# Kernel tuning notes

Measured on AMD Instinct MI355X. Metric: run time of the kernel, lower is better.

The kernel has to match this reference:

```python
import jax, jax.numpy as jnp
import numpy as np

IN_CH = 128
HID = 64
EPS = 1e-5
N_NODES = 20000
E_UND = 80000


def _build_line_graph(edge_index, num_nodes):
    # dedupe to unique undirected edges (src<dst); line-graph nodes = these edges
    src = np.asarray(edge_index[0]); dst = np.asarray(edge_index[1])
    m = src < dst
    u, v = src[m], dst[m]
    key = u.astype(np.int64) * num_nodes + v.astype(np.int64)
    _, first = np.unique(key, return_index=True)
    u, v = u[first], v[first]
    E = u.shape[0]
    # incidence lists grouped by node; all ordered pairs of co-incident edges
    nodes = np.concatenate([u, v])
    eids = np.concatenate([np.arange(E), np.arange(E)])
    order = np.argsort(nodes, kind="stable")
    nodes_s, eids_s = nodes[order], eids[order]
    counts = np.bincount(nodes_s, minlength=num_nodes)
    offsets = np.concatenate([np.zeros(1, np.int64), np.cumsum(counts)])
    grp_start = offsets[nodes_s]
    reps = counts[nodes_s]
    total = int(reps.sum())
    starts = np.cumsum(reps) - reps
    idx = np.arange(total) - np.repeat(starts, reps) + np.repeat(grp_start, reps)
    row = np.repeat(eids_s, reps); col = eids_s[idx]
    keep = row != col
    return np.stack([u, v]), np.stack([row[keep], col[keep]])


def _gcn_conv(x, src, dst, W, b):
    # PyG GCNConv: add self loops, symmetric D^-1/2 (A+I) D^-1/2 normalization
    N = x.shape[0]
    sl = jnp.arange(N)
    s = jnp.concatenate([src, sl]); d = jnp.concatenate([dst, sl])
    deg = jax.ops.segment_sum(jnp.ones(s.shape[0], x.dtype), d, num_segments=N)
    dinv = jax.lax.rsqrt(jnp.maximum(deg, 1.0))
    h = x @ W
    msg = h[s] * (dinv[s] * dinv[d])[:, None]
    return jax.ops.segment_sum(msg, d, num_segments=N) + b


def _edge_scores(line_x, lsrc, ldst, W1, b1, gamma1, beta1, W2, b2):
    h = _gcn_conv(line_x, lsrc, ldst, W1, b1)
    mu = h.mean(0); var = h.var(0)  # BatchNorm1d, training-mode batch stats
    h = jax.nn.relu(gamma1 * (h - mu) * jax.lax.rsqrt(var + EPS) + beta1)
    return jax.nn.sigmoid(_gcn_conv(h, lsrc, ldst, W2, b2))[:, 0]


def _cluster(clean, topk_idx, num_nodes):
    ti = np.asarray(topk_idx)
    sel_src = np.asarray(clean[0])[ti]; sel_dst = np.asarray(clean[1])[ti]
    n2c = np.arange(num_nodes)
    rev = sel_dst[::-1]
    _, fi = np.unique(rev, return_index=True)
    last = sel_dst.shape[0] - 1 - fi
    n2c[sel_dst[last]] = sel_src[last]
    uniq = np.unique(n2c)
    M = int(uniq.shape[0])
    old_to_new = np.full(num_nodes, -1, np.int64)
    old_to_new[uniq] = np.arange(M)
    return old_to_new[n2c], uniq, M


def _make_graph():
    rng = np.random.default_rng(0)
    a = rng.integers(0, N_NODES, E_UND)
    off = rng.integers(1, N_NODES, E_UND)
    b = (a + off) % N_NODES  # no self loops
    u = np.minimum(a, b); v = np.maximum(a, b)
    return np.stack([np.concatenate([u, v]), np.concatenate([v, u])]).astype(np.int64)


def _make_params():
    ks = jax.random.split(jax.random.key(0), 4)
    x = jax.random.normal(ks[0], (N_NODES, IN_CH), jnp.float32)
    W1 = jax.random.normal(ks[1], (IN_CH, HID), jnp.float32) / np.float32(np.sqrt(IN_CH))
    b1 = jnp.zeros((HID,), jnp.float32)
    gamma1 = jnp.ones((HID,), jnp.float32)
    beta1 = jnp.zeros((HID,), jnp.float32)
    W2 = jax.random.normal(ks[2], (HID, 1), jnp.float32) / np.float32(np.sqrt(HID))
    b2 = jnp.zeros((1,), jnp.float32)
    return x, W1, b1, gamma1, beta1, W2, b2


def setup_inputs() -> dict:
    x, W1, b1, gamma1, beta1, W2, b2 = _make_params()
    return {
        "x": x, "W1": W1, "b1": b1, "gamma1": gamma1, "beta1": beta1,
        "W2": W2, "b2": b2,
        "edge_index": jnp.asarray(_make_graph()),
        "batch": jnp.zeros((N_NODES,), jnp.int32),
    }


def reference(x, W1, b1, gamma1, beta1, W2, b2, edge_index, batch):
    N = x.shape[0]
    clean, line_ei = _build_line_graph(edge_index, N)
    csrc = jnp.asarray(clean[0]); cdst = jnp.asarray(clean[1])
    lsrc = jnp.asarray(line_ei[0]); ldst = jnp.asarray(line_ei[1])
    line_x = 0.5 * (x[csrc] + x[cdst])  # line-graph node features
    scores = _edge_scores(line_x, lsrc, ldst, W1, b1, gamma1, beta1, W2, b2)
    E_c = scores.shape[0]
    k = max(1, min(E_c // 2, N // 2))
    _, topk_idx = jax.lax.top_k(scores, k)
    new_indices, uniq, M = _cluster(clean, topk_idx, N)
    ni = jnp.asarray(new_indices)
    # aggregate: per-cluster mean of member node features (code's weights are unused)
    counts = jax.ops.segment_sum(jnp.ones(N, x.dtype), ni, num_segments=M)
    x_pool = jax.ops.segment_sum(x, ni, num_segments=M) / counts[:, None]
    batch_pool = batch[jnp.asarray(uniq)]
    # build_new_edges: relabel, drop self loops, coalesce (sorted unique)
    ei = np.asarray(edge_index)
    ns = new_indices[ei[0]]; nd = new_indices[ei[1]]
    keep = ns != nd
    pk = ns[keep] * M + nd[keep]
    upk = np.unique(pk)
    edge_index_pool = jnp.asarray(np.stack([upk // M, upk % M]))
    return (x_pool, edge_index_pool, batch_pool, scores, ni)
```

## Files before the change

kernel.cpp:

```cpp
#include <hip/hip_runtime.h>
#include <stdint.h>

typedef unsigned long long u64;
typedef unsigned int u32;

#define NND 20000
#define EUA 160000
#define EFE 80000
#define ICH 128
#define HIDC 64
#define SCAN_BS 256
#define NB_N ((NND + 255) / 256)
#define NB_EU ((EUA + 255) / 256)
#define NB_EF ((EFE + 255) / 256)
#define NB_E64 ((EFE * HIDC + 255) / 256)
#define NSCAN_B ((NND + SCAN_BS - 1) / SCAN_BS)
#define HIST_BLOCKS 128
#define GEB 64
#define XS_PAD 132
#define NCHAIN 4096
#define BK64 64
#define SEL_BINS 4096


__global__ void kScanA(const int* __restrict__ in, int* __restrict__ out,
                       int* __restrict__ bsums, int n) {
    __shared__ int sh[SCAN_BS];
    int tid = threadIdx.x;
    int i = blockIdx.x * SCAN_BS + tid;
    int v = (i < n) ? in[i] : 0;
    sh[tid] = v;
    __syncthreads();
    for (int o = 1; o < SCAN_BS; o <<= 1) {
        int t = (tid >= o) ? sh[tid - o] : 0;
        __syncthreads();
        sh[tid] += t;
        __syncthreads();
    }
    if (i < n) out[i] = sh[tid] - v;
    if (tid == SCAN_BS - 1) bsums[blockIdx.x] = sh[tid];
}
__global__ void kScanB(int* __restrict__ out, const int* __restrict__ bsums,
                       int n, int nb, int* __restrict__ totalDst) {
    __shared__ int sh[160];
    int tid = threadIdx.x;
    if (tid <= nb) sh[tid] = (tid < nb) ? bsums[tid] : 0;
    __syncthreads();
    if (tid == 0) {
        int acc = 0;
        for (int i = 0; i < nb; i++) { int t = sh[i]; sh[i] = acc; acc += t; }
        sh[nb] = acc;
    }
    __syncthreads();
    int i = blockIdx.x * SCAN_BS + tid;
    if (i < n) out[i] += sh[blockIdx.x];
    if (i == 0) {
        int tot = sh[nb];
        out[n] = tot;
        *totalDst = tot;
    }
}

__global__ void kFilterScatter64(const int* __restrict__ ei, int* __restrict__ cnt,
                                 int* __restrict__ bucketV) {
    int i = blockIdx.x * 256 + threadIdx.x;
    if (i >= EUA) return;
    int s = ei[i], d = ei[EUA + i];
    if (s < d) {
        int p = atomicAdd(&cnt[s], 1);
        bucketV[(s << 6) + p] = d;
    }
}
__global__ void kRankSort64(const int* __restrict__ in, int* __restrict__ out,
                            const int* __restrict__ lenA, int* __restrict__ ucnt) {
    int a = blockIdx.x;
    int len = lenA[a];
    int base = a << 6;
    for (int j = threadIdx.x; j < len; j += 64) {
        int v = in[base + j];
        int r = 0;
        for (int i = 0; i < len; i++) {
            int w = in[base + i];
            r += (w < v) || (w == v && i < j);
        }
        out[base + r] = v;
    }
    __syncthreads();
    int c = 0;
    for (int j = threadIdx.x; j < len; j += 64)
        c += (j == 0) || (out[base + j] != out[base + j - 1]);
#pragma unroll
    for (int o = 32; o > 0; o >>= 1) c += __shfl_down(c, o, 64);
    if (threadIdx.x == 0) ucnt[a] = c;
}
__global__ void kCompactInc(const int* __restrict__ arr, const int* __restrict__ cnt,
                            const int* __restrict__ uoff, int* __restrict__ eU,
                            int* __restrict__ eV, int* __restrict__ icnt) {
    int u = blockIdx.x * 256 + threadIdx.x;
    if (u >= NND) return;
    int s = u << 6, e = s + cnt[u], o = uoff[u];
    int myc = 0;
    for (int i = s; i < e; i++)
        if (i == s || arr[i] != arr[i - 1]) {
            int v = arr[i];
            eU[o] = u; eV[o] = v; o++;
            atomicAdd(&icnt[v], 1);
            myc++;
        }
    if (myc) atomicAdd(&icnt[u], myc);
}

__global__ void kIncScatterDinv64(const int* __restrict__ eU, const int* __restrict__ eV,
                                  const int* __restrict__ scal, int* __restrict__ itmp,
                                  int* __restrict__ ilist, const int* __restrict__ icnt,
                                  float* __restrict__ dinv) {
    int e = blockIdx.x * 256 + threadIdx.x;
    if (e >= scal[0]) return;
    int u = eU[e], v = eV[e];
    ilist[(u << 6) + atomicAdd(&itmp[u], 1)] = e;
    ilist[(v << 6) + atomicAdd(&itmp[v], 1)] = e;
    dinv[e] = rsqrtf((float)(icnt[u] + icnt[v] - 1));
}

__global__ void kGemm(const float* __restrict__ x, const float* __restrict__ W1,
                      const int* __restrict__ eU, const int* __restrict__ eV,
                      const int* __restrict__ scal, float* __restrict__ h) {
    __shared__ float W1s[ICH][HIDC];
    __shared__ float xs[GEB][XS_PAD];
    int t = threadIdx.x;
    int E = scal[0];
    int e0 = blockIdx.x * GEB;
    if (e0 >= E) return;

    {
        const float4* Wv = (const float4*)W1;
        float4* Ws = (float4*)&W1s[0][0];
        for (int i = t; i < ICH * HIDC / 4; i += 256) Ws[i] = Wv[i];
    }
    {
        int eb = t >> 2, q = t & 3;
        int e = e0 + eb;
        if (e < E) {
            int u = eU[e], v = eV[e];
            const float4* xu = (const float4*)(x + (size_t)u * ICH) + q * 8;
            const float4* xv = (const float4*)(x + (size_t)v * ICH) + q * 8;
            float* xd = &xs[eb][q * 32];
#pragma unroll
            for (int i = 0; i < 8; i++) {
                float4 a = xu[i], b = xv[i];
                xd[i * 4 + 0] = 0.5f * (a.x + b.x);
                xd[i * 4 + 1] = 0.5f * (a.y + b.y);
                xd[i * 4 + 2] = 0.5f * (a.z + b.z);
                xd[i * 4 + 3] = 0.5f * (a.w + b.w);
            }
        }
    }
    __syncthreads();

    int cg4 = (t & 15) * 4;
    int es = t >> 4;
    float a00=0,a01=0,a02=0,a03=0, a10=0,a11=0,a12=0,a13=0;
    float a20=0,a21=0,a22=0,a23=0, a30=0,a31=0,a32=0,a33=0;
#pragma unroll 4
    for (int k = 0; k < ICH; k++) {
        float4 wv = *(const float4*)&W1s[k][cg4];
        float x0 = xs[es][k], x1 = xs[es + 16][k];
        float x2 = xs[es + 32][k], x3 = xs[es + 48][k];
        a00 += x0 * wv.x; a01 += x0 * wv.y; a02 += x0 * wv.z; a03 += x0 * wv.w;
        a10 += x1 * wv.x; a11 += x1 * wv.y; a12 += x1 * wv.z; a13 += x1 * wv.w;
        a20 += x2 * wv.x; a21 += x2 * wv.y; a22 += x2 * wv.z; a23 += x2 * wv.w;
        a30 += x3 * wv.x; a31 += x3 * wv.y; a32 += x3 * wv.z; a33 += x3 * wv.w;
    }
    int e;
    e = e0 + es;
    if (e < E) *(float4*)&h[(size_t)e * HIDC + cg4] = make_float4(a00, a01, a02, a03);
    e = e0 + es + 16;
    if (e < E) *(float4*)&h[(size_t)e * HIDC + cg4] = make_float4(a10, a11, a12, a13);
    e = e0 + es + 32;
    if (e < E) *(float4*)&h[(size_t)e * HIDC + cg4] = make_float4(a20, a21, a22, a23);
    e = e0 + es + 48;
    if (e < E) *(float4*)&h[(size_t)e * HIDC + cg4] = make_float4(a30, a31, a32, a33);
}

__global__ void kSGather(const float* __restrict__ h, const float* __restrict__ dinv,
                         const int* __restrict__ icnt, const int* __restrict__ ilist,
                         float* __restrict__ S) {
    int n = blockIdx.x;
    int c = threadIdx.x;
    int base = n << 6, len = icnt[n];
    float acc = 0.f;
    for (int j = 0; j < len; j++) {
        int ed = ilist[base + j];
        acc += h[(size_t)ed * HIDC + c] * dinv[ed];
    }
    S[(size_t)n * HIDC + c] = acc;
}
__global__ void kConv1Red1(const float* __restrict__ h, const float* __restrict__ S,
                           const float* __restrict__ dinv, const int* __restrict__ eU,
                           const int* __restrict__ eV, const float* __restrict__ b1,
                           const int* __restrict__ scal, float* __restrict__ h2,
                           float* __restrict__ partial, float* __restrict__ partial2) {
    int t = threadIdx.x;
    int g = blockIdx.x * 4 + (t >> 6);
    int c = t & 63;
    int E = scal[0];
    float bc = b1[c];
    float acc = 0.f, acc2 = 0.f;
    for (int e = g; e < E; e += NCHAIN) {
        float a = dinv[e];
        float v = a * (S[(size_t)eU[e] * HIDC + c] + S[(size_t)eV[e] * HIDC + c]) -
                  a * a * h[(size_t)e * HIDC + c] + bc;
        h2[(size_t)e * HIDC + c] = v;
        acc += v;
        acc2 += v * v;
    }
    partial[g * HIDC + c] = acc;
    partial2[g * HIDC + c] = acc2;
}
__global__ void kRed2(const float* __restrict__ partial, const float* __restrict__ partial2,
                      const int* __restrict__ scal, float* __restrict__ muvar) {
    __shared__ float sh[4][HIDC];
    __shared__ float sh2[4][HIDC];
    int t = threadIdx.x;
    int q = t >> 6, c = t & 63;
    float acc = 0.f, acc2 = 0.f;
    int g0 = q * (NCHAIN / 4);
    for (int g = g0; g < g0 + NCHAIN / 4; g++) {
        acc += partial[g * HIDC + c];
        acc2 += partial2[g * HIDC + c];
    }
    sh[q][c] = acc;
    sh2[q][c] = acc2;
    __syncthreads();
    if (q == 0) {
        float Ef = (float)scal[0];
        float mu = (((sh[0][c] + sh[1][c]) + sh[2][c]) + sh[3][c]) / Ef;
        float m2 = (((sh2[0][c] + sh2[1][c]) + sh2[2][c]) + sh2[3][c]) / Ef;
        muvar[c] = mu;
        muvar[HIDC + c] = m2 - mu * mu;
    }
}
__global__ void kNormZ(const float* __restrict__ h2, const float* __restrict__ muvar,
                       const float* __restrict__ gamma1, const float* __restrict__ beta1,
                       const float* __restrict__ W2, const int* __restrict__ scal,
                       float* __restrict__ z) {
    int idx = blockIdx.x * 256 + threadIdx.x;
    int e = idx >> 6;
    if (e >= scal[0]) return;
    int c = idx & 63;
    float t = gamma1[c] * (h2[idx] - muvar[c]) * rsqrtf(muvar[HIDC + c] + 1e-5f) + beta1[c];
    t = t > 0.f ? t : 0.f;
    float p = t * W2[c];
#pragma unroll
    for (int o = 32; o > 0; o >>= 1) p += __shfl_down(p, o, 64);
    if (c == 0) z[e] = p;
}
__global__ void kS2(const float* __restrict__ z, const float* __restrict__ dinv,
                    const int* __restrict__ icnt, const int* __restrict__ ilist,
                    float* __restrict__ S2) {
    int n = blockIdx.x * 256 + threadIdx.x;
    if (n >= NND) return;
    int base = n << 6, len = icnt[n];
    float acc = 0.f;
    for (int j = 0; j < len; j++) {
        int e = ilist[base + j];
        acc += z[e] * dinv[e];
    }
    S2[n] = acc;
}
__global__ void kScore(const float* __restrict__ z, const float* __restrict__ S2,
                       const float* __restrict__ dinv, const int* __restrict__ eU,
                       const int* __restrict__ eV, const float* __restrict__ b2,
                       const int* __restrict__ scal, float* __restrict__ score,
                       u64* __restrict__ okey, u64* __restrict__ minOkey,
                       int* __restrict__ hist0) {
    __shared__ int sh[SEL_BINS];
    int t = threadIdx.x;
    for (int j = t; j < SEL_BINS; j += 256) sh[j] = 0;
    __syncthreads();
    int e = blockIdx.x * 256 + t;
    if (e < NND) minOkey[e] = ~0ULL;
    int E = scal[0];
    if (e < E) {
        float a = dinv[e];
        float l = a * (S2[eU[e]] + S2[eV[e]]) - a * a * z[e] + b2[0];
        float s = 1.f / (1.f + expf(-l));
        score[e] = s;
        u32 b = __float_as_uint(s);
        b = (b >> 31) ? ~b : (b | 0x80000000u);
        u64 key = (((u64)b) << 17) | (u32)(0x1FFFFu - (u32)e);
        okey[e] = key;
        atomicAdd(&sh[(int)((key >> 36) & (SEL_BINS - 1))], 1);
    }
    __syncthreads();
    for (int j = t; j < SEL_BINS; j += 256) {
        int v = sh[j];
        if (v) atomicAdd(&hist0[j], v);
    }
}

__device__ __forceinline__ u64 selReplay(const int* __restrict__ histBase, int passes,
                                         int E, int t, int* aux, int* shTmp) {
    int kr = E / 2;
    if (kr > NND / 2) kr = NND / 2;
    if (kr < 1) kr = 1;
    u64 pref = 1ULL << 48;
    for (int q = 0; q < passes; q++) {
        int shift = 36 - 12 * q;
        const int* hq = histBase + q * SEL_BINS;
        int b[16];
        int g = 0;
#pragma unroll
        for (int j = 0; j < 16; j++) { b[j] = hq[16 * t + j]; g += b[j]; }
        aux[t] = g;
        __syncthreads();
        for (int o = 1; o < 256; o <<= 1) {
            int v = (t + o < 256) ? aux[t + o] : 0;
            __syncthreads();
            aux[t] += v;
            __syncthreads();
        }
        int suf = aux[t] - g;
        if (suf < kr && kr <= suf + g) {
            int cum = suf, found = 16 * t;
            for (int j = 15; j >= 0; j--) {
                int hc = b[j];
                if (cum + hc >= kr) { found = 16 * t + j; break; }
                cum += hc;
            }
            shTmp[0] = found;
            shTmp[1] = kr - cum;
        }
        __syncthreads();
        pref |= ((u64)shTmp[0]) << shift;
        kr = shTmp[1];
        __syncthreads();
    }
    return pref;
}
__global__ void kHistR(const u64* __restrict__ okey, const int* __restrict__ scal,
                       int* __restrict__ histBase, int pass) {
    __shared__ int sh[4][SEL_BINS];
    __shared__ int aux[256];
    __shared__ int shTmp[2];
    int t = threadIdx.x;
    int E = scal[0];
    u64 p = selReplay(histBase, pass, E, t, aux, shTmp);
    for (int j = t; j < 4 * SEL_BINS; j += 256) ((int*)sh)[j] = 0;
    __syncthreads();
    int wv = t >> 6;
    int shift = 36 - 12 * pass;
    u64 maskHi = (~0ULL) << (shift + 12);
    for (int e = blockIdx.x * 256 + t; e < E; e += HIST_BLOCKS * 256) {
        u64 kk = okey[e];
        if ((kk & maskHi) == p)
            atomicAdd(&sh[wv][(int)((kk >> shift) & (SEL_BINS - 1))], 1);
    }
    __syncthreads();
    int* hp = histBase + pass * SEL_BINS;
    for (int j = t; j < SEL_BINS; j += 256) {
        int v = sh[0][j] + sh[1][j] + sh[2][j] + sh[3][j];
        if (v) atomicAdd(&hp[j], v);
    }
}

__global__ void kMinKey(const u64* __restrict__ okey, const int* __restrict__ eV,
                        const int* __restrict__ scal, const int* __restrict__ histBase,
                        u64* __restrict__ minOkey) {
    __shared__ int aux[256];
    __shared__ int shTmp[2];
    int t = threadIdx.x;
    int E = scal[0];
    u64 pref = selReplay(histBase, 4, E, t, aux, shTmp);
    int i = blockIdx.x * 256 + t;
    if (i < E) {
        u64 k = okey[i];
        if (k >= pref) atomicMin(&minOkey[eV[i]], k);
    }
}
__global__ void kCluster(const u64* __restrict__ minOkey, const int* __restrict__ eU,
                         int* __restrict__ n2c, int* __restrict__ present,
                         int* __restrict__ csize, int* __restrict__ cmemb) {
    int v = blockIdx.x * 256 + threadIdx.x;
    if (v >= NND) return;
    u64 mk = minOkey[v];
    int m = v;
    if (mk != ~0ULL) m = eU[0x1FFFFu - (u32)(mk & 0x1FFFFu)];
    n2c[v] = m;
    present[m] = 1;
    int slot = atomicAdd(&csize[m], 1);
    cmemb[(m << 6) + slot] = v;
}

__global__ void kXPoolCE(const float* __restrict__ x, const int* __restrict__ n2c,
                         const int* __restrict__ o2n, const int* __restrict__ present,
                         const int* __restrict__ csize, const int* __restrict__ cmemb,
                         const int* __restrict__ ei, int* __restrict__ ni,
                         float* __restrict__ dout, int* __restrict__ ecnt2) {
    int u = blockIdx.x;
    int c = threadIdx.x;
    int gid = u * 128 + c;
    if (gid < EUA) {
        int a = o2n[n2c[ei[gid]]], b = o2n[n2c[ei[EUA + gid]]];
        if (a != b) atomicAdd(&ecnt2[a], 1);
    }
    if (c == 0) ni[u] = o2n[n2c[u]];
    if (!present[u]) return;
    int s = csize[u];
    int base = u << 6;
    float acc = 0.f;
    for (int j = 0; j < s; j++)
        acc += x[(size_t)cmemb[base + j] * ICH + c];
    dout[(size_t)o2n[u] * ICH + c] = acc / (float)s;
}

__global__ void kCEscatter(const int* __restrict__ ei, const int* __restrict__ ni,
                           const int* __restrict__ eoff2, int* __restrict__ etmp2,
                           int* __restrict__ bkD) {
    int i = blockIdx.x * 256 + threadIdx.x;
    if (i >= EUA) return;
    int a = ni[ei[i]], b = ni[ei[EUA + i]];
    if (a != b) {
        int p = eoff2[a] + atomicAdd(&etmp2[a], 1);
        bkD[p] = b;
    }
}
__global__ void kRankSort(const int* __restrict__ in, int* __restrict__ out,
                          const int* __restrict__ offA, int* __restrict__ ucnt) {
    int a = blockIdx.x;
    int s = offA[a], e = offA[a + 1], len = e - s;
    for (int j = threadIdx.x; j < len; j += 64) {
        int v = in[s + j];
        int r = 0;
        for (int i = 0; i < len; i++) {
            int w = in[s + i];
            r += (w < v) || (w == v && i < j);
        }
        out[s + r] = v;
    }
    __syncthreads();
    int c = 0;
    for (int j = threadIdx.x; j < len; j += 64)
        c += (j == 0) || (out[s + j] != out[s + j - 1]);
#pragma unroll
    for (int o = 32; o > 0; o >>= 1) c += __shfl_down(c, o, 64);
    if (threadIdx.x == 0) ucnt[a] = c;
}
__global__ void kCEwriteTail(const int* __restrict__ bkD2, const int* __restrict__ eoff2,
                             const int* __restrict__ ueoff, const int* __restrict__ scal,
                             const int* __restrict__ batch, const int* __restrict__ present,
                             const int* __restrict__ o2n, const float* __restrict__ score,
                             const int* __restrict__ ni, float* __restrict__ dout) {
    int i = blockIdx.x * 256 + threadIdx.x;
    int E = scal[0], M = scal[2], Ep = scal[3];
    size_t base = (size_t)M * ICH;
    if (i < NND) {
        int s = eoff2[i], e = eoff2[i + 1];
        float* r0 = dout + base;
        float* r1 = r0 + Ep;
        int o = ueoff[i];
        for (int j = s; j < e; j++)
            if (j == s || bkD2[j] != bkD2[j - 1]) {
                r0[o] = (float)i;
                r1[o] = (float)bkD2[j];
                o++;
            }
    }
    size_t tb = base + 2 * (size_t)Ep;
    if (i < NND && present[i]) dout[tb + o2n[i]] = (float)batch[i];
    if (i < E) dout[tb + M + i] = score[i];
    if (i < NND) dout[tb + M + E + i] = (float)ni[i];
}

extern "C" void kernel_launch(void* const* d_in, const int* in_sizes, int n_in,
                              void* d_out, int out_size, void* d_ws, size_t ws_size,
                              hipStream_t stream) {
    (void)in_sizes; (void)n_in; (void)ws_size; (void)out_size;
    const float* x = (const float*)d_in[0];
    const float* W1 = (const float*)d_in[1];
    const float* b1 = (const float*)d_in[2];
    const float* gamma1 = (const float*)d_in[3];
    const float* beta1 = (const float*)d_in[4];
    const float* W2 = (const float*)d_in[5];
    const float* b2 = (const float*)d_in[6];
    const int* ei = (const int*)d_in[7];
    const int* batch = (const int*)d_in[8];
    float* dout = (float*)d_out;

    char* w = (char*)d_ws;
    size_t off = 0;
    auto carve = [&](size_t bytes) -> void* {
        off = (off + 255) & ~(size_t)255;
        void* p = w + off;
        off += bytes;
        return p;
    };
    char* zero0 = w;
    int* cnt = (int*)carve(NND * 4);
    int* itmp = (int*)carve(NND * 4);
    int* icnt = (int*)carve(NND * 4);
    int* present = (int*)carve(NND * 4);
    int* csize = (int*)carve(NND * 4);
    int* ecnt2 = (int*)carve(NND * 4);
    int* etmp2 = (int*)carve(NND * 4);
    int* scal = (int*)carve(16 * 4);
    int* hist4 = (int*)carve((size_t)4 * SEL_BINS * 4);
    size_t zeroBytes = off;
    int* ucnt = (int*)carve(NND * 4);
    int* uoff = (int*)carve((NND + 2) * 4);
    int* bsums = (int*)carve((NSCAN_B + 2) * 4);
    int* n2c = (int*)carve(NND * 4);
    int* o2n = (int*)carve((NND + 2) * 4);
    int* niArr = (int*)carve(NND * 4);
    int* eoff2 = (int*)carve((NND + 2) * 4);
    int* uecnt = (int*)carve(NND * 4);
    int* ueoff = (int*)carve((NND + 2) * 4);
    int* bucketV = (int*)carve((size_t)NND * BK64 * 4);
    int* bucketS = (int*)carve((size_t)NND * BK64 * 4);
    int* eU = (int*)carve(EFE * 4);
    int* eV = (int*)carve(EFE * 4);
    int* ilist = (int*)carve((size_t)NND * BK64 * 4);
    int* ilistS = (int*)carve((size_t)NND * BK64 * 4);
    int* bkD = (int*)carve(EUA * 4);
    int* bkD2 = (int*)carve(EUA * 4);
    u64* okey = (u64*)carve(EFE * 8);
    u64* minOkey = (u64*)carve(NND * 8);
    float* dinv = (float*)carve(EFE * 4);
    float* h = (float*)carve((size_t)EFE * HIDC * 4);
    float* h2 = (float*)carve((size_t)EFE * HIDC * 4);
    float* Snode = (float*)carve((size_t)NND * HIDC * 4);
    float* partial = (float*)carve((size_t)NCHAIN * HIDC * 4);
    float* partial2 = (float*)carve((size_t)NCHAIN * HIDC * 4);
    float* muvar = (float*)carve(128 * 4);
    float* zArr = (float*)carve(EFE * 4);
    float* S2 = (float*)carve(NND * 4);
    float* score = (float*)carve(EFE * 4);

    auto scan = [&](const int* in, int* outp, int* totalDst) {
        kScanA<<<NSCAN_B, SCAN_BS, 0, stream>>>(in, outp, bsums, NND);
        kScanB<<<NSCAN_B, SCAN_BS, 0, stream>>>(outp, bsums, NND, NSCAN_B, totalDst);
    };

    hipMemsetAsync(zero0, 0, zeroBytes, stream);

    kFilterScatter64<<<NB_EU, 256, 0, stream>>>(ei, cnt, bucketV);
    kRankSort64<<<NND, 64, 0, stream>>>(bucketV, bucketS, cnt, ucnt);
    scan(ucnt, uoff, scal + 0);
    kCompactInc<<<NB_N, 256, 0, stream>>>(bucketS, cnt, uoff, eU, eV, icnt);

    kIncScatterDinv64<<<NB_EF, 256, 0, stream>>>(eU, eV, scal, itmp, ilist, icnt, dinv);
    kRankSort64<<<NND, 64, 0, stream>>>(ilist, ilistS, icnt, ucnt);

    kGemm<<<(EFE + GEB - 1) / GEB, 256, 0, stream>>>(x, W1, eU, eV, scal, h);
    kSGather<<<NND, HIDC, 0, stream>>>(h, dinv, icnt, ilistS, Snode);
    kConv1Red1<<<NCHAIN / 4, 256, 0, stream>>>(h, Snode, dinv, eU, eV, b1, scal, h2,
                                               partial, partial2);
    kRed2<<<1, 256, 0, stream>>>(partial, partial2, scal, muvar);
    kNormZ<<<NB_E64, 256, 0, stream>>>(h2, muvar, gamma1, beta1, W2, scal, zArr);

    kS2<<<NB_N, 256, 0, stream>>>(zArr, dinv, icnt, ilistS, S2);
    kScore<<<NB_EF, 256, 0, stream>>>(zArr, S2, dinv, eU, eV, b2, scal, score, okey,
                                      minOkey, hist4);

    for (int p = 1; p < 4; p++)
        kHistR<<<HIST_BLOCKS, 256, 0, stream>>>(okey, scal, hist4, p);

    kMinKey<<<NB_EF, 256, 0, stream>>>(okey, eV, scal, hist4, minOkey);
    kCluster<<<NB_N, 256, 0, stream>>>(minOkey, eU, n2c, present, csize, bucketV);
    scan(present, o2n, scal + 2);

    kXPoolCE<<<NND, 128, 0, stream>>>(x, n2c, o2n, present, csize, bucketV, ei,
                                      niArr, dout, ecnt2);

    scan(ecnt2, eoff2, scal + 4);
    kCEscatter<<<NB_EU, 256, 0, stream>>>(ei, niArr, eoff2, etmp2, bkD);
    kRankSort<<<NND, 64, 0, stream>>>(bkD, bkD2, eoff2, uecnt);
    scan(uecnt, ueoff, scal + 3);
    kCEwriteTail<<<NB_EF, 256, 0, stream>>>(bkD2, eoff2, ueoff, scal, batch, present,
                                            o2n, score, niArr, dout);
}
```

Measured before the change: 360.4 us.

## Fold scan second pass into consumers and merge gemm with incidence sort

Each two-kernel scan is replaced by a single block-local scan whose totals are added atomically. Every consumer rebuilds the block prefix in shared memory and adds it on the fly. Incidence-list scatter is folded into the compaction kernel, and dinv plus the incidence rank-sort are merged into the GEMM launch as extra blocks. The one-block BN reduction becomes an 8-block producer/consumer ring reduction, with the final mean and variance computed in the norm kernel. This removes several launches and serial phases, but adds redundant prefix rebuilding in every block and intra-block spin-waits.

```diff
diff --git a/kernel.cpp b/kernel.cpp
--- a/kernel.cpp
+++ b/kernel.cpp
@@ -15,20 +15,23 @@
 #define NB_EF ((EFE + 255) / 256)
 #define NB_E64 ((EFE * HIDC + 255) / 256)
 #define NSCAN_B ((NND + SCAN_BS - 1) / SCAN_BS)
+#define PRE_N (NSCAN_B + 1)
 #define HIST_BLOCKS 128
 #define GEB 64
+#define GEMM_BLKS ((EFE + GEB - 1) / GEB)
+#define SORT_BLKS 1250
 #define XS_PAD 132
 #define NCHAIN 4096
 #define BK64 64
 #define SEL_BINS 4096
 
 
-__global__ void kScanA(const int* __restrict__ in, int* __restrict__ out,
-                       int* __restrict__ bsums, int n) {
+__global__ void kScanA2(const int* __restrict__ in, int* __restrict__ out,
+                        int* __restrict__ bsums, int* __restrict__ totalDst) {
     __shared__ int sh[SCAN_BS];
     int tid = threadIdx.x;
     int i = blockIdx.x * SCAN_BS + tid;
-    int v = (i < n) ? in[i] : 0;
+    int v = (i < NND) ? in[i] : 0;
     sh[tid] = v;
     __syncthreads();
     for (int o = 1; o < SCAN_BS; o <<= 1) {
@@ -37,28 +40,24 @@
         sh[tid] += t;
         __syncthreads();
     }
-    if (i < n) out[i] = sh[tid] - v;
-    if (tid == SCAN_BS - 1) bsums[blockIdx.x] = sh[tid];
-}
-__global__ void kScanB(int* __restrict__ out, const int* __restrict__ bsums,
-                       int n, int nb, int* __restrict__ totalDst) {
-    __shared__ int sh[160];
-    int tid = threadIdx.x;
-    if (tid <= nb) sh[tid] = (tid < nb) ? bsums[tid] : 0;
-    __syncthreads();
-    if (tid == 0) {
-        int acc = 0;
-        for (int i = 0; i < nb; i++) { int t = sh[i]; sh[i] = acc; acc += t; }
-        sh[nb] = acc;
-    }
-    __syncthreads();
-    int i = blockIdx.x * SCAN_BS + tid;
-    if (i < n) out[i] += sh[blockIdx.x];
-    if (i == 0) {
-        int tot = sh[nb];
-        out[n] = tot;
-        *totalDst = tot;
-    }
+    if (i <= NND) out[i] = sh[tid] - v;
+    if (tid == SCAN_BS - 1) {
+        bsums[blockIdx.x] = sh[tid];
+        atomicAdd(totalDst, sh[tid]);
+    }
+}
+__device__ __forceinline__ void buildPre(const int* __restrict__ bsums,
+                                         int* pre, int t, int nthr) {
+    for (int k = t; k < NSCAN_B; k += nthr) pre[k + 1] = bsums[k];
+    if (t == 0) pre[0] = 0;
+    __syncthreads();
+    if (t == 0)
+        for (int k = 1; k <= NSCAN_B; k++) pre[k] += pre[k - 1];
+    __syncthreads();
+}
+__device__ __forceinline__ int scanAt(const int* __restrict__ raw,
+                                      const int* pre, int i) {
+    return raw[i] + pre[i >> 8];
 }
 
 __global__ void kFilterScatter64(const int* __restrict__ ei, int* __restrict__ cnt,
@@ -93,45 +92,65 @@
     for (int o = 32; o > 0; o >>= 1) c += __shfl_down(c, o, 64);
     if (threadIdx.x == 0) ucnt[a] = c;
 }
-__global__ void kCompactInc(const int* __restrict__ arr, const int* __restrict__ cnt,
-                            const int* __restrict__ uoff, int* __restrict__ eU,
-                            int* __restrict__ eV, int* __restrict__ icnt) {
-    int u = blockIdx.x * 256 + threadIdx.x;
+__global__ void kCompactInc2(const int* __restrict__ arr, const int* __restrict__ cnt,
+                             const int* __restrict__ uoffRaw,
+                             const int* __restrict__ bsumsH,
+                             int* __restrict__ eU, int* __restrict__ eV,
+                             int* __restrict__ icnt, int* __restrict__ itmp,
+                             int* __restrict__ ilist) {
+    __shared__ int pre[PRE_N];
+    int t = threadIdx.x;
+    buildPre(bsumsH, pre, t, 256);
+    int u = blockIdx.x * 256 + t;
     if (u >= NND) return;
-    int s = u << 6, e = s + cnt[u], o = uoff[u];
+    int s = u << 6, e = s + cnt[u];
+    int o = scanAt(uoffRaw, pre, u);
     int myc = 0;
     for (int i = s; i < e; i++)
         if (i == s || arr[i] != arr[i - 1]) {
             int v = arr[i];
-            eU[o] = u; eV[o] = v; o++;
+            eU[o] = u; eV[o] = v;
+            ilist[(u << 6) + atomicAdd(&itmp[u], 1)] = o;
+            ilist[(v << 6) + atomicAdd(&itmp[v], 1)] = o;
             atomicAdd(&icnt[v], 1);
-            myc++;
+            o++; myc++;
         }
     if (myc) atomicAdd(&icnt[u], myc);
 }
 
-__global__ void kIncScatterDinv64(const int* __restrict__ eU, const int* __restrict__ eV,
-                                  const int* __restrict__ scal, int* __restrict__ itmp,
-                                  int* __restrict__ ilist, const int* __restrict__ icnt,
-                                  float* __restrict__ dinv) {
-    int e = blockIdx.x * 256 + threadIdx.x;
-    if (e >= scal[0]) return;
-    int u = eU[e], v = eV[e];
-    ilist[(u << 6) + atomicAdd(&itmp[u], 1)] = e;
-    ilist[(v << 6) + atomicAdd(&itmp[v], 1)] = e;
-    dinv[e] = rsqrtf((float)(icnt[u] + icnt[v] - 1));
-}
-
-__global__ void kGemm(const float* __restrict__ x, const float* __restrict__ W1,
-                      const int* __restrict__ eU, const int* __restrict__ eV,
-                      const int* __restrict__ scal, float* __restrict__ h) {
+__global__ void kGemmSort(const float* __restrict__ x, const float* __restrict__ W1,
+                          const int* __restrict__ eU, const int* __restrict__ eV,
+                          const int* __restrict__ scal, const int* __restrict__ icnt,
+                          float* __restrict__ dinv, float* __restrict__ h,
+                          const int* __restrict__ ilist, int* __restrict__ ilistS) {
     __shared__ float W1s[ICH][HIDC];
     __shared__ float xs[GEB][XS_PAD];
     int t = threadIdx.x;
     int E = scal[0];
+    if (blockIdx.x >= GEMM_BLKS) {
+        int w = t >> 6, c = t & 63;
+        for (int a = (blockIdx.x - GEMM_BLKS) * 4 + w; a < NND; a += SORT_BLKS * 4) {
+            int len = icnt[a];
+            int base = a << 6;
+            for (int j = c; j < len; j += 64) {
+                int v = ilist[base + j];
+                int r = 0;
+                for (int i = 0; i < len; i++) {
+                    int wv = ilist[base + i];
+                    r += (wv < v) || (wv == v && i < j);
+                }
+                ilistS[base + r] = v;
+            }
+        }
+        return;
+    }
+    {
+        int gid = blockIdx.x * 256 + t;
+        if (gid < E)
+            dinv[gid] = rsqrtf((float)(icnt[eU[gid]] + icnt[eV[gid]] - 1));
+    }
     int e0 = blockIdx.x * GEB;
     if (e0 >= E) return;
-
     {
         const float4* Wv = (const float4*)W1;
         float4* Ws = (float4*)&W1s[0][0];
@@ -217,38 +236,63 @@
     partial[g * HIDC + c] = acc;
     partial2[g * HIDC + c] = acc2;
 }
-__global__ void kRed2(const float* __restrict__ partial, const float* __restrict__ partial2,
-                      const int* __restrict__ scal, float* __restrict__ muvar) {
-    __shared__ float sh[4][HIDC];
-    __shared__ float sh2[4][HIDC];
-    int t = threadIdx.x;
-    int q = t >> 6, c = t & 63;
-    float acc = 0.f, acc2 = 0.f;
-    int g0 = q * (NCHAIN / 4);
-    for (int g = g0; g < g0 + NCHAIN / 4; g++) {
-        acc += partial[g * HIDC + c];
-        acc2 += partial2[g * HIDC + c];
-    }
-    sh[q][c] = acc;
-    sh2[q][c] = acc2;
-    __syncthreads();
-    if (q == 0) {
-        float Ef = (float)scal[0];
-        float mu = (((sh[0][c] + sh[1][c]) + sh[2][c]) + sh[3][c]) / Ef;
-        float m2 = (((sh2[0][c] + sh2[1][c]) + sh2[2][c]) + sh2[3][c]) / Ef;
-        muvar[c] = mu;
-        muvar[HIDC + c] = m2 - mu * mu;
-    }
-}
-__global__ void kNormZ(const float* __restrict__ h2, const float* __restrict__ muvar,
-                       const float* __restrict__ gamma1, const float* __restrict__ beta1,
-                       const float* __restrict__ W2, const int* __restrict__ scal,
-                       float* __restrict__ z) {
+__global__ void kRed2a(const float* __restrict__ partial,
+                       const float* __restrict__ partial2,
+                       float* __restrict__ miniP) {
+    __shared__ float ring[2][64][HIDC];
+    __shared__ int doneCnt[2];
+    __shared__ int freeTok[2];
+    int t = threadIdx.x, b = blockIdx.x;
+    int w = t >> 6, c = t & 63;
+    int q = b & 3;
+    const float* src = ((b & 4) ? partial2 : partial) +
+                       (size_t)q * (NCHAIN / 4) * HIDC;
+    if (t == 0) { doneCnt[0] = 0; doneCnt[1] = 0; freeTok[0] = 0; freeTok[1] = 1; }
+    __syncthreads();
+    if (w == 0) {
+        float acc = 0.f;
+        for (int ch = 0; ch < 16; ch++) {
+            int slot = ch & 1;
+            int need = 192 * ((ch >> 1) + 1);
+            while (__atomic_load_n(&doneCnt[slot], __ATOMIC_RELAXED) < need)
+                ;
+            const float* rg = &ring[slot][0][0];
+            for (int r = 0; r < 64; r++) acc += rg[r * HIDC + c];
+            asm volatile("s_waitcnt lgkmcnt(0)" ::: "memory");
+            __atomic_store_n(&freeTok[slot], ch + 2, __ATOMIC_RELAXED);
+        }
+        miniP[b * HIDC + c] = acc;
+    } else {
+        int p = t - 64;
+        for (int ch = 0; ch < 16; ch++) {
+            int slot = ch & 1;
+            while (__atomic_load_n(&freeTok[slot], __ATOMIC_RELAXED) < ch)
+                ;
+            const float* sbase = src + (size_t)(ch * 64) * HIDC;
+            for (int idx = p; idx < 64 * 16; idx += 192) {
+                int row = idx >> 4, c4 = (idx & 15) << 2;
+                float4 v = *(const float4*)(sbase + row * HIDC + c4);
+                *(float4*)&ring[slot][row][c4] = v;
+            }
+            asm volatile("s_waitcnt vmcnt(0) lgkmcnt(0)" ::: "memory");
+            __atomic_fetch_add(&doneCnt[slot], 1, __ATOMIC_RELAXED);
+        }
+    }
+}
+__global__ void kNormZ2(const float* __restrict__ h2, const float* __restrict__ miniP,
+                        const float* __restrict__ gamma1, const float* __restrict__ beta1,
+                        const float* __restrict__ W2, const int* __restrict__ scal,
+                        float* __restrict__ z) {
     int idx = blockIdx.x * 256 + threadIdx.x;
     int e = idx >> 6;
     if (e >= scal[0]) return;
     int c = idx & 63;
-    float t = gamma1[c] * (h2[idx] - muvar[c]) * rsqrtf(muvar[HIDC + c] + 1e-5f) + beta1[c];
+    float Ef = (float)scal[0];
+    float mu = (((miniP[0 * HIDC + c] + miniP[1 * HIDC + c]) +
+                 miniP[2 * HIDC + c]) + miniP[3 * HIDC + c]) / Ef;
+    float m2 = (((miniP[4 * HIDC + c] + miniP[5 * HIDC + c]) +
+                 miniP[6 * HIDC + c]) + miniP[7 * HIDC + c]) / Ef;
+    float t = gamma1[c] * (h2[idx] - mu) * rsqrtf(m2 - mu * mu + 1e-5f) + beta1[c];
     t = t > 0.f ? t : 0.f;
     float p = t * W2[c];
 #pragma unroll
@@ -363,7 +407,6 @@
         if (v) atomicAdd(&hp[j], v);
     }
 }
-
 __global__ void kMinKey(const u64* __restrict__ okey, const int* __restrict__ eV,
                         const int* __restrict__ scal, const int* __restrict__ histBase,
                         u64* __restrict__ minOkey) {
@@ -392,44 +435,57 @@
     cmemb[(m << 6) + slot] = v;
 }
 
-__global__ void kXPoolCE(const float* __restrict__ x, const int* __restrict__ n2c,
-                         const int* __restrict__ o2n, const int* __restrict__ present,
-                         const int* __restrict__ csize, const int* __restrict__ cmemb,
-                         const int* __restrict__ ei, int* __restrict__ ni,
-                         float* __restrict__ dout, int* __restrict__ ecnt2) {
+__global__ void kXPoolCE2(const float* __restrict__ x, const int* __restrict__ n2c,
+                          const int* __restrict__ o2nRaw, const int* __restrict__ bsumsA,
+                          const int* __restrict__ present, const int* __restrict__ csize,
+                          const int* __restrict__ cmemb, const int* __restrict__ ei,
+                          int* __restrict__ ni, float* __restrict__ dout,
+                          int* __restrict__ ecnt2) {
+    __shared__ int pre[PRE_N];
     int u = blockIdx.x;
     int c = threadIdx.x;
+    buildPre(bsumsA, pre, c, 128);
     int gid = u * 128 + c;
     if (gid < EUA) {
-        int a = o2n[n2c[ei[gid]]], b = o2n[n2c[ei[EUA + gid]]];
+        int a = scanAt(o2nRaw, pre, n2c[ei[gid]]);
+        int b = scanAt(o2nRaw, pre, n2c[ei[EUA + gid]]);
         if (a != b) atomicAdd(&ecnt2[a], 1);
     }
-    if (c == 0) ni[u] = o2n[n2c[u]];
+    if (c == 0) ni[u] = scanAt(o2nRaw, pre, n2c[u]);
     if (!present[u]) return;
     int s = csize[u];
     int base = u << 6;
     float acc = 0.f;
     for (int j = 0; j < s; j++)
         acc += x[(size_t)cmemb[base + j] * ICH + c];
-    dout[(size_t)o2n[u] * ICH + c] = acc / (float)s;
-}
-
-__global__ void kCEscatter(const int* __restrict__ ei, const int* __restrict__ ni,
-                           const int* __restrict__ eoff2, int* __restrict__ etmp2,
-                           int* __restrict__ bkD) {
-    int i = blockIdx.x * 256 + threadIdx.x;
+    dout[(size_t)scanAt(o2nRaw, pre, u) * ICH + c] = acc / (float)s;
+}
+
+__global__ void kCEscatter2(const int* __restrict__ ei, const int* __restrict__ ni,
+                            const int* __restrict__ eoff2Raw,
+                            const int* __restrict__ bsumsB,
+                            int* __restrict__ etmp2, int* __restrict__ bkD) {
+    __shared__ int pre[PRE_N];
+    int t = threadIdx.x;
+    buildPre(bsumsB, pre, t, 256);
+    int i = blockIdx.x * 256 + t;
     if (i >= EUA) return;
     int a = ni[ei[i]], b = ni[ei[EUA + i]];
     if (a != b) {
-        int p = eoff2[a] + atomicAdd(&etmp2[a], 1);
+        int p = scanAt(eoff2Raw, pre, a) + atomicAdd(&etmp2[a], 1);
         bkD[p] = b;
     }
 }
-__global__ void kRankSort(const int* __restrict__ in, int* __restrict__ out,
-                          const int* __restrict__ offA, int* __restrict__ ucnt) {
+__global__ void kRankSort2(const int* __restrict__ in, int* __restrict__ out,
+                           const int* __restrict__ eoff2Raw,
+                           const int* __restrict__ bsumsB, int* __restrict__ ucnt) {
+    __shared__ int pre[PRE_N];
+    int t = threadIdx.x;
+    buildPre(bsumsB, pre, t, 64);
     int a = blockIdx.x;
-    int s = offA[a], e = offA[a + 1], len = e - s;
-    for (int j = threadIdx.x; j < len; j += 64) {
+    int s = scanAt(eoff2Raw, pre, a), e = scanAt(eoff2Raw, pre, a + 1);
+    int len = e - s;
+    for (int j = t; j < len; j += 64) {
         int v = in[s + j];
         int r = 0;
         for (int i = 0; i < len; i++) {
@@ -440,25 +496,50 @@
     }
     __syncthreads();
     int c = 0;
-    for (int j = threadIdx.x; j < len; j += 64)
+    for (int j = t; j < len; j += 64)
         c += (j == 0) || (out[s + j] != out[s + j - 1]);
 #pragma unroll
     for (int o = 32; o > 0; o >>= 1) c += __shfl_down(c, o, 64);
-    if (threadIdx.x == 0) ucnt[a] = c;
-}
-__global__ void kCEwriteTail(const int* __restrict__ bkD2, const int* __restrict__ eoff2,
-                             const int* __restrict__ ueoff, const int* __restrict__ scal,
-                             const int* __restrict__ batch, const int* __restrict__ present,
-                             const int* __restrict__ o2n, const float* __restrict__ score,
-                             const int* __restrict__ ni, float* __restrict__ dout) {
-    int i = blockIdx.x * 256 + threadIdx.x;
+    if (t == 0) ucnt[a] = c;
+}
+__global__ void kCEwriteTail2(const int* __restrict__ bkD2,
+                              const int* __restrict__ eoff2Raw,
+                              const int* __restrict__ ueoffRaw,
+                              const int* __restrict__ o2nRaw,
+                              const int* __restrict__ bsumsA,
+                              const int* __restrict__ bsumsB,
+                              const int* __restrict__ bsumsC,
+                              const int* __restrict__ scal,
+                              const int* __restrict__ batch,
+                              const int* __restrict__ present,
+                              const float* __restrict__ score,
+                              const int* __restrict__ ni, float* __restrict__ dout) {
+    __shared__ int preA[PRE_N];
+    __shared__ int preB[PRE_N];
+    __shared__ int preC[PRE_N];
+    int t = threadIdx.x;
+    for (int k = t; k < NSCAN_B; k += 256) {
+        preA[k + 1] = bsumsA[k];
+        preB[k + 1] = bsumsB[k];
+        preC[k + 1] = bsumsC[k];
+    }
+    if (t == 0) { preA[0] = 0; preB[0] = 0; preC[0] = 0; }
+    __syncthreads();
+    if (t == 0)
+        for (int k = 1; k <= NSCAN_B; k++) {
+            preA[k] += preA[k - 1];
+            preB[k] += preB[k - 1];
+            preC[k] += preC[k - 1];
+        }
+    __syncthreads();
+    int i = blockIdx.x * 256 + t;
     int E = scal[0], M = scal[2], Ep = scal[3];
     size_t base = (size_t)M * ICH;
     if (i < NND) {
-        int s = eoff2[i], e = eoff2[i + 1];
+        int s = scanAt(eoff2Raw, preB, i), e = scanAt(eoff2Raw, preB, i + 1);
         float* r0 = dout + base;
         float* r1 = r0 + Ep;
-        int o = ueoff[i];
+        int o = scanAt(ueoffRaw, preC, i);
         for (int j = s; j < e; j++)
             if (j == s || bkD2[j] != bkD2[j - 1]) {
                 r0[o] = (float)i;
@@ -467,7 +548,7 @@
             }
     }
     size_t tb = base + 2 * (size_t)Ep;
-    if (i < NND && present[i]) dout[tb + o2n[i]] = (float)batch[i];
+    if (i < NND && present[i]) dout[tb + scanAt(o2nRaw, preA, i)] = (float)batch[i];
     if (i < E) dout[tb + M + i] = score[i];
     if (i < NND) dout[tb + M + E + i] = (float)ni[i];
 }
@@ -508,7 +589,10 @@
     size_t zeroBytes = off;
     int* ucnt = (int*)carve(NND * 4);
     int* uoff = (int*)carve((NND + 2) * 4);
-    int* bsums = (int*)carve((NSCAN_B + 2) * 4);
+    int* bsumsH = (int*)carve((NSCAN_B + 2) * 4);
+    int* bsumsA = (int*)carve((NSCAN_B + 2) * 4);
+    int* bsumsB = (int*)carve((NSCAN_B + 2) * 4);
+    int* bsumsC = (int*)carve((NSCAN_B + 2) * 4);
     int* n2c = (int*)carve(NND * 4);
     int* o2n = (int*)carve((NND + 2) * 4);
     int* niArr = (int*)carve(NND * 4);
@@ -531,51 +615,48 @@
     float* Snode = (float*)carve((size_t)NND * HIDC * 4);
     float* partial = (float*)carve((size_t)NCHAIN * HIDC * 4);
     float* partial2 = (float*)carve((size_t)NCHAIN * HIDC * 4);
-    float* muvar = (float*)carve(128 * 4);
+    float* miniP = (float*)carve(8 * HIDC * 4);
     float* zArr = (float*)carve(EFE * 4);
     float* S2 = (float*)carve(NND * 4);
     float* score = (float*)carve(EFE * 4);
 
-    auto scan = [&](const int* in, int* outp, int* totalDst) {
-        kScanA<<<NSCAN_B, SCAN_BS, 0, stream>>>(in, outp, bsums, NND);
-        kScanB<<<NSCAN_B, SCAN_BS, 0, stream>>>(outp, bsums, NND, NSCAN_B, totalDst);
-    };
-
     hipMemsetAsync(zero0, 0, zeroBytes, stream);
 
     kFilterScatter64<<<NB_EU, 256, 0, stream>>>(ei, cnt, bucketV);
     kRankSort64<<<NND, 64, 0, stream>>>(bucketV, bucketS, cnt, ucnt);
-    scan(ucnt, uoff, scal + 0);
-    kCompactInc<<<NB_N, 256, 0, stream>>>(bucketS, cnt, uoff, eU, eV, icnt);
-
-    kIncScatterDinv64<<<NB_EF, 256, 0, stream>>>(eU, eV, scal, itmp, ilist, icnt, dinv);
-    kRankSort64<<<NND, 64, 0, stream>>>(ilist, ilistS, icnt, ucnt);
-
-    kGemm<<<(EFE + GEB - 1) / GEB, 256, 0, stream>>>(x, W1, eU, eV, scal, h);
+    kScanA2<<<NSCAN_B, SCAN_BS, 0, stream>>>(ucnt, uoff, bsumsH, scal + 0);
+    kCompactInc2<<<NB_N, 256, 0, stream>>>(bucketS, cnt, uoff, bsumsH, eU, eV,
+                                           icnt, itmp, ilist);
+
+    kGemmSort<<<GEMM_BLKS + SORT_BLKS, 256, 0, stream>>>(x, W1, eU, eV, scal,
+                                                         icnt, dinv, h, ilist,
+                                                         ilistS);
+
     kSGather<<<NND, HIDC, 0, stream>>>(h, dinv, icnt, ilistS, Snode);
-    kConv1Red1<<<NCHAIN / 4, 256, 0, stream>>>(h, Snode, dinv, eU, eV, b1, scal, h2,
-                                               partial, partial2);
-    kRed2<<<1, 256, 0, stream>>>(partial, partial2, scal, muvar);
-    kNormZ<<<NB_E64, 256, 0, stream>>>(h2, muvar, gamma1, beta1, W2, scal, zArr);
+    kConv1Red1<<<NCHAIN / 4, 256, 0, stream>>>(h, Snode, dinv, eU, eV, b1, scal,
+                                               h2, partial, partial2);
+    kRed2a<<<8, 256, 0, stream>>>(partial, partial2, miniP);
+    kNormZ2<<<NB_E64, 256, 0, stream>>>(h2, miniP, gamma1, beta1, W2, scal, zArr);
 
     kS2<<<NB_N, 256, 0, stream>>>(zArr, dinv, icnt, ilistS, S2);
-    kScore<<<NB_EF, 256, 0, stream>>>(zArr, S2, dinv, eU, eV, b2, scal, score, okey,
-                                      minOkey, hist4);
+    kScore<<<NB_EF, 256, 0, stream>>>(zArr, S2, dinv, eU, eV, b2, scal, score,
+                                      okey, minOkey, hist4);
 
     for (int p = 1; p < 4; p++)
         kHistR<<<HIST_BLOCKS, 256, 0, stream>>>(okey, scal, hist4, p);
 
     kMinKey<<<NB_EF, 256, 0, stream>>>(okey, eV, scal, hist4, minOkey);
     kCluster<<<NB_N, 256, 0, stream>>>(minOkey, eU, n2c, present, csize, bucketV);
-    scan(present, o2n, scal + 2);
-
-    kXPoolCE<<<NND, 128, 0, stream>>>(x, n2c, o2n, present, csize, bucketV, ei,
-                                      niArr, dout, ecnt2);
-
-    scan(ecnt2, eoff2, scal + 4);
-    kCEscatter<<<NB_EU, 256, 0, stream>>>(ei, niArr, eoff2, etmp2, bkD);
-    kRankSort<<<NND, 64, 0, stream>>>(bkD, bkD2, eoff2, uecnt);
-    scan(uecnt, ueoff, scal + 3);
-    kCEwriteTail<<<NB_EF, 256, 0, stream>>>(bkD2, eoff2, ueoff, scal, batch, present,
-                                            o2n, score, niArr, dout);
-}
+    kScanA2<<<NSCAN_B, SCAN_BS, 0, stream>>>(present, o2n, bsumsA, scal + 2);
+
+    kXPoolCE2<<<NND, 128, 0, stream>>>(x, n2c, o2n, bsumsA, present, csize,
+                                       bucketV, ei, niArr, dout, ecnt2);
+
+    kScanA2<<<NSCAN_B, SCAN_BS, 0, stream>>>(ecnt2, eoff2, bsumsB, scal + 15);
+    kCEscatter2<<<NB_EU, 256, 0, stream>>>(ei, niArr, eoff2, bsumsB, etmp2, bkD);
+    kRankSort2<<<NND, 64, 0, stream>>>(bkD, bkD2, eoff2, bsumsB, uecnt);
+    kScanA2<<<NSCAN_B, SCAN_BS, 0, stream>>>(uecnt, ueoff, bsumsC, scal + 3);
+    kCEwriteTail2<<<NB_EF, 256, 0, stream>>>(bkD2, eoff2, ueoff, o2n, bsumsA,
+                                             bsumsB, bsumsC, scal, batch, present,
+                                             score, niArr, dout);
+}
```

New measurement: 382.1 us. 6.0% more time.
